# Kernel optimization log

Measured on AMD Instinct MI355X. Metric: run time of the kernel, lower is better.

The kernel has to match this reference:

```python
import jax, jax.numpy as jnp
import numpy as np

EMBED_DIM = 1024
N1 = 4096
N2 = 4096


def setup_inputs() -> dict:
    key = jax.random.key(0)
    ks = jax.random.split(key, 14)
    s = 1.0 / np.sqrt(EMBED_DIM)
    def lin(k):
        kw, kb = jax.random.split(k)
        W = jax.random.uniform(kw, (EMBED_DIM, EMBED_DIM), jnp.float32, -s, s)
        b = jax.random.uniform(kb, (EMBED_DIM,), jnp.float32, -s, s)
        return W, b
    Wq1, bq1 = lin(ks[0]); Wk1, bk1 = lin(ks[1]); Wv1, bv1 = lin(ks[2])
    Wq2, bq2 = lin(ks[3]); Wk2, bk2 = lin(ks[4]); Wv2, bv2 = lin(ks[5])
    x1 = jax.random.normal(ks[6], (N1, EMBED_DIM), jnp.float32)
    x2 = jax.random.normal(ks[7], (N2, EMBED_DIM), jnp.float32)
    return {
        "input_tensor1": x1, "input_tensor2": x2,
        "Wq1": Wq1, "bq1": bq1, "Wk1": Wk1, "bk1": bk1, "Wv1": Wv1, "bv1": bv1,
        "Wq2": Wq2, "bq2": bq2, "Wk2": Wk2, "bk2": bk2, "Wv2": Wv2, "bv2": bv2,
    }


def reference(input_tensor1, input_tensor2,
              Wq1, bq1, Wk1, bk1, Wv1, bv1,
              Wq2, bq2, Wk2, bk2, Wv2, bv2):
    scale = 1.0 / jnp.sqrt(jnp.asarray(EMBED_DIM, input_tensor1.dtype))
    # torch Linear: y = x @ W.T + b
    q1 = input_tensor1 @ Wq1.T + bq1   # [N1, D]
    k1 = input_tensor1 @ Wk1.T + bk1
    v1 = input_tensor1 @ Wv1.T + bv1
    q2 = input_tensor2 @ Wq2.T + bq2   # [N2, D]
    k2 = input_tensor2 @ Wk2.T + bk2
    v2 = input_tensor2 @ Wv2.T + bv2
    # stream-2 queries attend over stream-1 keys/values
    scores1 = (q2 @ k1.T) * scale                  # [N2, N1]
    probs1 = jax.nn.softmax(scores1, axis=-1)      # dropout p=0 -> identity
    context1 = probs1 @ v1                         # [N2, D]
    # stream-1 queries attend over stream-2 keys/values
    scores2 = (q1 @ k2.T) * scale                  # [N1, N2]
    probs2 = jax.nn.softmax(scores2, axis=-1)
    context2 = probs2 @ v2                         # [N1, D]
    return (context1, context2)
```

## Files before the change

kernel.cpp:

```cpp
#include <hip/hip_runtime.h>
#include <hip/hip_bf16.h>
#include <cstdint>
#include <cstddef>

#define DEVINL __device__ __forceinline__

typedef __attribute__((ext_vector_type(4))) float   f32x4;
typedef __bf16 bf16x8 __attribute__((ext_vector_type(8)));
typedef __attribute__((ext_vector_type(4))) short   short4v;
typedef __attribute__((ext_vector_type(4))) float   float4v;

static constexpr int DIM = 1024;
static constexpr int NTOK = 4096;

DEVINL unsigned short f2bf(float f) {
  unsigned u = __float_as_uint(f);
  u += 0x7FFF + ((u >> 16) & 1);
  return (unsigned short)(u >> 16);
}
DEVINL float bf2f(unsigned short s) {
  return __uint_as_float(((unsigned)s) << 16);
}

DEVINL void gll16(const void* g, void* l) {
  __builtin_amdgcn_global_load_lds(
      (const __attribute__((address_space(1))) void*)g,
      (__attribute__((address_space(3))) void*)l, 16, 0, 0);
}

struct B3 { int bx, by, bz; };
DEVINL B3 xcd_remap(int GX, int GY, int GZ) {
  const int flat = blockIdx.x + GX * (blockIdx.y + GY * blockIdx.z);
  const int nwg  = GX * GY * GZ;
  const int chunk = nwg >> 3;
  const int vbid = (flat & 7) * chunk + (flat >> 3);
  B3 r;
  r.bx = vbid % GX;
  r.by = (vbid / GX) % GY;
  r.bz = vbid / (GX * GY);
  return r;
}

DEVINL void core256x128(const unsigned short* __restrict__ A, int lda,
                        const unsigned short* __restrict__ B, int ldb,
                        int K, int brow, int bcol, f32x4 acc[4][4])
{
  __shared__ unsigned short lds[73728];
  const int t = threadIdx.x;
  const int w = t >> 6, l = t & 63;
  const int wr = w >> 1, wc = w & 1;
  const int l15 = l & 15;
  const int scol = ((l & 3) ^ ((l >> 3) & 3)) << 3;
  const int cs   = (((l >> 4) ^ ((l15 >> 1) & 3)) << 3);

  const unsigned short* aL = A + (size_t)(brow * 256 + w * 16 + (l >> 2)) * lda + scol;
  const unsigned short* bL = B + (size_t)(bcol * 128 + w * 16 + (l >> 2)) * ldb + scol;

#pragma unroll
  for (int m = 0; m < 4; ++m)
#pragma unroll
    for (int n = 0; n < 4; ++n) {
      f32x4 z = {0.f, 0.f, 0.f, 0.f};
      acc[m][n] = z;
    }

#define STAGE(buf, kt)                                                         \
  {                                                                            \
    gll16(aL + (size_t)(kt) * 32,                                              \
          lds + (buf) * 12288 + w * 512);                                      \
    gll16(aL + (size_t)128 * lda + (size_t)(kt) * 32,                          \
          lds + (buf) * 12288 + 4096 + w * 512);                               \
    gll16(bL + (size_t)(kt) * 32,                                              \
          lds + (buf) * 12288 + 8192 + w * 512);                               \
  }

  const int NT = K >> 5;

  STAGE(0, 0); STAGE(1, 1); STAGE(2, 2); STAGE(3, 3);

  bf16x8 af[4], bfv[4];
  int cur = 0;
  for (int kt = 0; kt < NT; ++kt) {
    int st = cur + 4; if (st >= 6) st -= 6;
    if (kt + 4 < NT) STAGE(st, kt + 4);

    const int rem = NT - 1 - kt;
    if (rem >= 4)      asm volatile("s_waitcnt vmcnt(12)" ::: "memory");
    else if (rem == 3) asm volatile("s_waitcnt vmcnt(9)"  ::: "memory");
    else if (rem == 2) asm volatile("s_waitcnt vmcnt(6)"  ::: "memory");
    else if (rem == 1) asm volatile("s_waitcnt vmcnt(3)"  ::: "memory");
    else               asm volatile("s_waitcnt vmcnt(0)"  ::: "memory");
    asm volatile("" ::: "memory");
    __builtin_amdgcn_s_barrier();
    asm volatile("" ::: "memory");

    const unsigned short* base = lds + cur * 12288;
#pragma unroll
    for (int m = 0; m < 4; ++m)
      af[m] = *(const bf16x8*)(base + (wr * 64 + m * 16 + l15) * 32 + cs);
#pragma unroll
    for (int n = 0; n < 4; ++n)
      bfv[n] = *(const bf16x8*)(base + 8192 + (wc * 64 + n * 16 + l15) * 32 + cs);

    __builtin_amdgcn_s_setprio(1);
#pragma unroll
    for (int m = 0; m < 4; ++m)
#pragma unroll
      for (int n = 0; n < 4; ++n)
        acc[m][n] = __builtin_amdgcn_mfma_f32_16x16x32_bf16(af[m], bfv[n], acc[m][n], 0, 0, 0);
    __builtin_amdgcn_s_setprio(0);

    cur = (cur + 1 == 6) ? 0 : cur + 1;
  }
#undef STAGE
}

__global__ __launch_bounds__(512, 2)
void gemm_scores(const unsigned short* __restrict__ A,
                 const unsigned short* __restrict__ B,
                 unsigned short* __restrict__ S, float scale)
{
  const B3 b = xcd_remap(32, 16, 1);
  f32x4 acc[4][4];
  core256x128(A, DIM, B, DIM, DIM, b.by, b.bx, acc);

  const int t = threadIdx.x, w = t >> 6, l = t & 63;
  const int wr = w >> 1, wc = w & 1;
  const int rr = (l >> 4) * 4, cc = l & 15;
#pragma unroll
  for (int m = 0; m < 4; ++m) {
    const int row0 = b.by * 256 + wr * 64 + m * 16 + rr;
#pragma unroll
    for (int n = 0; n < 4; ++n) {
      const int col = b.bx * 128 + wc * 64 + n * 16 + cc;
#pragma unroll
      for (int i = 0; i < 4; ++i)
        S[(size_t)(row0 + i) * NTOK + col] = f2bf(acc[m][n][i] * scale);
    }
  }
}

__global__ __launch_bounds__(512, 2)
void qkv_gemm(const unsigned short* __restrict__ x1, const unsigned short* __restrict__ x2,
              const unsigned short* __restrict__ W6,
              const float* bq1, const float* bk1, const float* bv1,
              const float* bq2, const float* bk2, const float* bv2,
              unsigned short* q1, unsigned short* k1, unsigned short* v1T,
              unsigned short* q2, unsigned short* k2, unsigned short* v2T)
{
  const B3 b = xcd_remap(8, 16, 6);
  const int g = b.bz;
  const unsigned short* A = (g < 3) ? x1 : x2;
  const unsigned short* W = W6 + (size_t)g * (DIM * DIM);
  const float* bias = (g == 0) ? bq1 : (g == 1) ? bk1 : (g == 2) ? bv1
                    : (g == 3) ? bq2 : (g == 4) ? bk2 : bv2;
  unsigned short* out = (g == 0) ? q1 : (g == 1) ? k1 : (g == 2) ? v1T
                      : (g == 3) ? q2 : (g == 4) ? k2 : v2T;
  const bool vT = (g == 2 || g == 5);

  f32x4 acc[4][4];
  core256x128(A, DIM, W, DIM, DIM, b.by, b.bx, acc);

  const int t = threadIdx.x, w = t >> 6, l = t & 63;
  const int wr = w >> 1, wc = w & 1;
  const int rr = (l >> 4) * 4, cc = l & 15;

  if (!vT) {
#pragma unroll
    for (int m = 0; m < 4; ++m) {
      const int row0 = b.by * 256 + wr * 64 + m * 16 + rr;
#pragma unroll
      for (int n = 0; n < 4; ++n) {
        const int col = b.bx * 128 + wc * 64 + n * 16 + cc;
        const float bv_ = bias[col];
#pragma unroll
        for (int i = 0; i < 4; ++i)
          out[(size_t)(row0 + i) * DIM + col] = f2bf(acc[m][n][i] + bv_);
      }
    }
  } else {
#pragma unroll
    for (int m = 0; m < 4; ++m) {
      const int row0 = b.by * 256 + wr * 64 + m * 16 + rr;
#pragma unroll
      for (int n = 0; n < 4; ++n) {
        const int col = b.bx * 128 + wc * 64 + n * 16 + cc;
        const float bv_ = bias[col];
        short4v pk;
#pragma unroll
        for (int i = 0; i < 4; ++i) pk[i] = (short)f2bf(acc[m][n][i] + bv_);
        *(short4v*)(out + (size_t)col * NTOK + row0) = pk;
      }
    }
  }
}

__global__ __launch_bounds__(512, 2)
void pv_gemm(const unsigned short* __restrict__ S1,
             const unsigned short* __restrict__ S2,
             const unsigned short* __restrict__ vTcat,
             float* __restrict__ out)
{
  const B3 b = xcd_remap(16, 16, 1);
  const int bx = b.bx, by = b.by;
  const unsigned short* A = (bx < 8) ? S1 : S2;

  f32x4 acc[4][4];
  core256x128(A, NTOK, vTcat, NTOK, NTOK, by, bx, acc);

  const int t = threadIdx.x, w = t >> 6, l = t & 63;
  const int wr = w >> 1, wc = w & 1;
  const int rr = (l >> 4) * 4, cc = l & 15;
#pragma unroll
  for (int m = 0; m < 4; ++m) {
    const int row0 = by * 256 + wr * 64 + m * 16 + rr;
#pragma unroll
    for (int n = 0; n < 4; ++n) {
      const int cg = bx * 128 + wc * 64 + n * 16 + cc;
      float* dstBase = (cg < 1024) ? (out + cg) : (out + 4194304 + (cg - 1024));
#pragma unroll
      for (int i = 0; i < 4; ++i)
        dstBase[(size_t)(row0 + i) * 1024] = acc[m][n][i];
    }
  }
}

__global__ __launch_bounds__(256)
void softmax_inplace(unsigned short* __restrict__ S)
{
  const int row = blockIdx.x;
  unsigned short* r = S + (size_t)row * NTOK;
  const int t = threadIdx.x, wave = t >> 6, lane = t & 63;
  __shared__ float red[4];

  bf16x8 d0 = *(const bf16x8*)(r + t * 8);
  bf16x8 d1 = *(const bf16x8*)(r + 2048 + t * 8);
  float v[16];
  {
    const unsigned short* p0 = (const unsigned short*)&d0;
    const unsigned short* p1 = (const unsigned short*)&d1;
#pragma unroll
    for (int j = 0; j < 8; ++j) { v[j] = bf2f(p0[j]); v[8 + j] = bf2f(p1[j]); }
  }
  float mx = v[0];
#pragma unroll
  for (int j = 1; j < 16; ++j) mx = fmaxf(mx, v[j]);
#pragma unroll
  for (int o = 32; o > 0; o >>= 1) mx = fmaxf(mx, __shfl_xor(mx, o));
  if (lane == 0) red[wave] = mx;
  __syncthreads();
  mx = fmaxf(fmaxf(red[0], red[1]), fmaxf(red[2], red[3]));

  float s = 0.f;
#pragma unroll
  for (int j = 0; j < 16; ++j) { v[j] = __expf(v[j] - mx); s += v[j]; }
#pragma unroll
  for (int o = 32; o > 0; o >>= 1) s += __shfl_xor(s, o);
  __syncthreads();
  if (lane == 0) red[wave] = s;
  __syncthreads();
  s = red[0] + red[1] + red[2] + red[3];
  const float inv = 1.0f / s;

  unsigned short o0[8], o1[8];
#pragma unroll
  for (int j = 0; j < 8; ++j) { o0[j] = f2bf(v[j] * inv); o1[j] = f2bf(v[8 + j] * inv); }
  *(bf16x8*)(r + t * 8)        = *(const bf16x8*)o0;
  *(bf16x8*)(r + 2048 + t * 8) = *(const bf16x8*)o1;
}

__global__ __launch_bounds__(256)
void cvt2(const float* __restrict__ a, const float* __restrict__ b,
          unsigned short* __restrict__ oa, unsigned short* __restrict__ ob)
{
  const float* in = blockIdx.y ? b : a;
  unsigned short* out = blockIdx.y ? ob : oa;
  const size_t i = ((size_t)blockIdx.x * 256 + threadIdx.x) * 4;
  float4v x = *(const float4v*)(in + i);
  short4v o;
#pragma unroll
  for (int j = 0; j < 4; ++j) o[j] = (short)f2bf(x[j]);
  *(short4v*)(out + i) = o;
}

__global__ __launch_bounds__(256)
void cvt_w(const float* w0, const float* w1, const float* w2,
           const float* w3, const float* w4, const float* w5,
           unsigned short* __restrict__ W6)
{
  const float* srcs[6] = {w0, w1, w2, w3, w4, w5};
  const float* in = srcs[blockIdx.y];
  unsigned short* out = W6 + (size_t)blockIdx.y * (DIM * DIM);
  const size_t i = ((size_t)blockIdx.x * 256 + threadIdx.x) * 4;
  float4v x = *(const float4v*)(in + i);
  short4v o;
#pragma unroll
  for (int j = 0; j < 4; ++j) o[j] = (short)f2bf(x[j]);
  *(short4v*)(out + i) = o;
}

extern "C" void kernel_launch(void* const* d_in, const int* in_sizes, int n_in,
                              void* d_out, int out_size, void* d_ws, size_t ws_size,
                              hipStream_t stream)
{
  const float* x1  = (const float*)d_in[0];
  const float* x2  = (const float*)d_in[1];
  const float* Wq1 = (const float*)d_in[2];  const float* bq1 = (const float*)d_in[3];
  const float* Wk1 = (const float*)d_in[4];  const float* bk1 = (const float*)d_in[5];
  const float* Wv1 = (const float*)d_in[6];  const float* bv1 = (const float*)d_in[7];
  const float* Wq2 = (const float*)d_in[8];  const float* bq2 = (const float*)d_in[9];
  const float* Wk2 = (const float*)d_in[10]; const float* bk2 = (const float*)d_in[11];
  const float* Wv2 = (const float*)d_in[12]; const float* bv2 = (const float*)d_in[13];
  float* out = (float*)d_out;

  unsigned short* ws  = (unsigned short*)d_ws;
  const size_t NTD = (size_t)NTOK * DIM;
  const size_t SM  = (size_t)NTOK * NTOK;
  unsigned short* x1b = ws;
  unsigned short* x2b = x1b + NTD;
  unsigned short* W6  = x2b + NTD;
  unsigned short* S1  = ws;
  unsigned short* S2  = ws + SM;
  unsigned short* q1  = ws + 2 * SM;
  unsigned short* k1  = q1 + NTD;
  unsigned short* q2  = k1 + NTD;
  unsigned short* k2  = q2 + NTD;
  unsigned short* vT  = k2 + NTD;
  unsigned short* v1T = vT;
  unsigned short* v2T = vT + NTD;

  const dim3 blk(256);
  cvt2 <<<dim3(NTD / 1024, 2), blk, 0, stream>>>(x1, x2, x1b, x2b);
  cvt_w<<<dim3((DIM * DIM) / 1024, 6), blk, 0, stream>>>(Wq1, Wk1, Wv1, Wq2, Wk2, Wv2, W6);

  qkv_gemm<<<dim3(8, 16, 6), dim3(512), 0, stream>>>(
      x1b, x2b, W6, bq1, bk1, bv1, bq2, bk2, bv2, q1, k1, v1T, q2, k2, v2T);

  const float scale = 0.03125f;

  gemm_scores<<<dim3(32, 16), dim3(512), 0, stream>>>(q2, k1, S1, scale);
  softmax_inplace<<<dim3(NTOK), blk, 0, stream>>>(S1);
  gemm_scores<<<dim3(32, 16), dim3(512), 0, stream>>>(q1, k2, S2, scale);
  softmax_inplace<<<dim3(NTOK), blk, 0, stream>>>(S2);

  pv_gemm<<<dim3(16, 16), dim3(512), 0, stream>>>(S1, S2, vT, out);
}
```

Baseline: 277.0 us.

## Use 256x256 tiled GEMM core with split-phase pipeline for QKV and scores

```diff
diff --git a/kernel.cpp b/kernel.cpp
--- a/kernel.cpp
+++ b/kernel.cpp
@@ -41,6 +41,125 @@
   return r;
 }
 
+DEVINL void core256v2(const unsigned short* __restrict__ A, int lda,
+                      const unsigned short* __restrict__ B, int ldb,
+                      int K, int brow, int bcol, f32x4 acc[8][4])
+{
+  __shared__ unsigned short lds[65536];
+  const int t = threadIdx.x;
+  const int w = t >> 6, l = t & 63;
+  const int wr = w >> 2, wc = w & 3;
+  const int srow = l >> 3;
+  const int scol = ((l & 7) ^ srow) << 3;
+  const int l15 = l & 15;
+  const int cs0 = (((l >> 4) << 3)        ^ ((l & 7) << 3));
+  const int cs1 = ((32 + ((l >> 4) << 3)) ^ ((l & 7) << 3));
+
+  const unsigned short* aL = A + (size_t)(brow * 256 + srow) * lda + scol;
+  const unsigned short* bL = B + (size_t)(bcol * 256 + srow) * ldb + scol;
+
+#pragma unroll
+  for (int m = 0; m < 8; ++m)
+#pragma unroll
+    for (int n = 0; n < 4; ++n) {
+      f32x4 z = {0.f, 0.f, 0.f, 0.f};
+      acc[m][n] = z;
+    }
+
+#define STA_(Sbase, h, r, kt)                                                  \
+  gll16(aL + (size_t)((r)*128 + (h)*64 + (w << 3)) * lda + (size_t)(kt)*64,    \
+        lds + (Sbase) + ((r)*128 + (h)*64 + (w << 3)) * 64)
+#define STB_(Sbase, h, r, kt)                                                  \
+  { const int g16_ = w + (r)*8;                                                \
+    const int r0_ = (g16_ >> 2)*64 + (h)*32 + (g16_ & 3)*8;                    \
+    gll16(bL + (size_t)r0_ * ldb + (size_t)(kt)*64, lds + (Sbase) + r0_ * 64); }
+#define LDA_(Abase, mh)                                                        \
+  _Pragma("unroll")                                                            \
+  for (int m4 = 0; m4 < 4; ++m4) {                                             \
+    const unsigned short* p_ = lds + (Abase) + (wr*128 + (mh)*64 + m4*16 + l15)*64; \
+    af[m4][0] = *(const bf16x8*)(p_ + cs0);                                    \
+    af[m4][1] = *(const bf16x8*)(p_ + cs1);                                    \
+  }
+#define LDB_(Bbase, nh)                                                        \
+  _Pragma("unroll")                                                            \
+  for (int n2 = 0; n2 < 2; ++n2) {                                             \
+    const unsigned short* p_ = lds + (Bbase) + (wc*64 + (nh)*32 + n2*16 + l15)*64;  \
+    bfr[n2][0] = *(const bf16x8*)(p_ + cs0);                                   \
+    bfr[n2][1] = *(const bf16x8*)(p_ + cs1);                                   \
+  }
+#define MF_(mh, nh)                                                            \
+  __builtin_amdgcn_s_setprio(1);                                               \
+  _Pragma("unroll")                                                            \
+  for (int m4 = 0; m4 < 4; ++m4)                                               \
+  _Pragma("unroll")                                                            \
+  for (int n2 = 0; n2 < 2; ++n2) {                                             \
+    f32x4 c_ = acc[(mh)*4 + m4][(nh)*2 + n2];                                  \
+    c_ = __builtin_amdgcn_mfma_f32_16x16x32_bf16(af[m4][0], bfr[n2][0], c_, 0,0,0); \
+    c_ = __builtin_amdgcn_mfma_f32_16x16x32_bf16(af[m4][1], bfr[n2][1], c_, 0,0,0); \
+    acc[(mh)*4 + m4][(nh)*2 + n2] = c_;                                        \
+  }                                                                            \
+  __builtin_amdgcn_s_setprio(0);
+#define VMW4() asm volatile("s_waitcnt vmcnt(4)" ::: "memory")
+#define VMW0() asm volatile("s_waitcnt vmcnt(0)" ::: "memory")
+#define BARR() do { asm volatile("" ::: "memory");                             \
+                    __builtin_amdgcn_s_barrier();                              \
+                    asm volatile("" ::: "memory"); } while (0)
+
+  STA_(0, 0, 0, 0); STA_(0, 0, 1, 0); STB_(16384, 0, 0, 0); STB_(16384, 0, 1, 0);
+  STA_(0, 1, 0, 0); STA_(0, 1, 1, 0); STB_(16384, 1, 0, 0); STB_(16384, 1, 1, 0);
+
+  bf16x8 af[4][2], bfr[2][2];
+  const int NT = K >> 6;
+  for (int kt = 0; kt < NT - 1; ++kt) {
+    const int Ab = (kt & 1) * 32768;
+    const int Bb = Ab + 16384;
+    const int Sa = ((kt & 1) ^ 1) * 32768;
+    const int Sb = Sa + 16384;
+
+    VMW4(); BARR();
+    STA_(Sa, 0, 0, kt + 1); STA_(Sa, 0, 1, kt + 1);
+    STB_(Sb, 0, 0, kt + 1); STB_(Sb, 0, 1, kt + 1);
+    LDA_(Ab, 0); LDB_(Bb, 0);
+    MF_(0, 0);
+
+    VMW4(); BARR();
+    STA_(Sa, 1, 0, kt + 1); STA_(Sa, 1, 1, kt + 1);
+    STB_(Sb, 1, 0, kt + 1); STB_(Sb, 1, 1, kt + 1);
+    LDA_(Ab, 1);
+    MF_(1, 0);
+
+    LDB_(Bb, 1);
+    MF_(1, 1);
+
+    LDA_(Ab, 0);
+    MF_(0, 1);
+  }
+
+  {
+    const int kt = NT - 1;
+    const int Ab = (kt & 1) * 32768;
+    const int Bb = Ab + 16384;
+    VMW4(); BARR();
+    LDA_(Ab, 0); LDB_(Bb, 0);
+    MF_(0, 0);
+    VMW0(); BARR();
+    LDA_(Ab, 1);
+    MF_(1, 0);
+    LDB_(Bb, 1);
+    MF_(1, 1);
+    LDA_(Ab, 0);
+    MF_(0, 1);
+  }
+#undef STA_
+#undef STB_
+#undef LDA_
+#undef LDB_
+#undef MF_
+#undef VMW4
+#undef VMW0
+#undef BARR
+}
+
 DEVINL void core256x128(const unsigned short* __restrict__ A, int lda,
                         const unsigned short* __restrict__ B, int ldb,
                         int K, int brow, int bcol, f32x4 acc[4][4])
@@ -115,40 +234,39 @@
 #undef STAGE
 }
 
-__global__ __launch_bounds__(512, 2)
-void gemm_scores(const unsigned short* __restrict__ A,
-                 const unsigned short* __restrict__ B,
-                 unsigned short* __restrict__ S, float scale)
-{
-  const B3 b = xcd_remap(32, 16, 1);
-  f32x4 acc[4][4];
-  core256x128(A, DIM, B, DIM, DIM, b.by, b.bx, acc);
+__global__ __launch_bounds__(512, 1)
+void gemm256_scores(const unsigned short* __restrict__ A,
+                    const unsigned short* __restrict__ B,
+                    unsigned short* __restrict__ S, float scale)
+{
+  const B3 b = xcd_remap(16, 16, 1);
+  f32x4 acc[8][4];
+  core256v2(A, DIM, B, DIM, DIM, b.by, b.bx, acc);
 
   const int t = threadIdx.x, w = t >> 6, l = t & 63;
-  const int wr = w >> 1, wc = w & 1;
-  const int rr = (l >> 4) * 4, cc = l & 15;
-#pragma unroll
-  for (int m = 0; m < 4; ++m) {
-    const int row0 = b.by * 256 + wr * 64 + m * 16 + rr;
-#pragma unroll
-    for (int n = 0; n < 4; ++n) {
-      const int col = b.bx * 128 + wc * 64 + n * 16 + cc;
+  const int wr = w >> 2, wc = w & 3;
+  const int r4 = (l >> 4) * 4, c = l & 15;
+  const int row0 = b.by * 256 + wr * 128;
+  const int col0 = b.bx * 256 + wc * 64;
+#pragma unroll
+  for (int mf = 0; mf < 8; ++mf)
+#pragma unroll
+    for (int nf = 0; nf < 4; ++nf)
 #pragma unroll
       for (int i = 0; i < 4; ++i)
-        S[(size_t)(row0 + i) * NTOK + col] = f2bf(acc[m][n][i] * scale);
-    }
-  }
-}
-
-__global__ __launch_bounds__(512, 2)
-void qkv_gemm(const unsigned short* __restrict__ x1, const unsigned short* __restrict__ x2,
-              const unsigned short* __restrict__ W6,
-              const float* bq1, const float* bk1, const float* bv1,
-              const float* bq2, const float* bk2, const float* bv2,
-              unsigned short* q1, unsigned short* k1, unsigned short* v1T,
-              unsigned short* q2, unsigned short* k2, unsigned short* v2T)
-{
-  const B3 b = xcd_remap(8, 16, 6);
+        S[(size_t)(row0 + mf*16 + r4 + i) * NTOK + col0 + nf*16 + c] =
+            f2bf(acc[mf][nf][i] * scale);
+}
+
+__global__ __launch_bounds__(512, 1)
+void qkv256(const unsigned short* __restrict__ x1, const unsigned short* __restrict__ x2,
+            const unsigned short* __restrict__ W6,
+            const float* bq1, const float* bk1, const float* bv1,
+            const float* bq2, const float* bk2, const float* bv2,
+            unsigned short* q1, unsigned short* k1, unsigned short* v1T,
+            unsigned short* q2, unsigned short* k2, unsigned short* v2T)
+{
+  const B3 b = xcd_remap(4, 16, 6);
   const int g = b.bz;
   const unsigned short* A = (g < 3) ? x1 : x2;
   const unsigned short* W = W6 + (size_t)g * (DIM * DIM);
@@ -158,40 +276,38 @@
                       : (g == 3) ? q2 : (g == 4) ? k2 : v2T;
   const bool vT = (g == 2 || g == 5);
 
-  f32x4 acc[4][4];
-  core256x128(A, DIM, W, DIM, DIM, b.by, b.bx, acc);
+  f32x4 acc[8][4];
+  core256v2(A, DIM, W, DIM, DIM, b.by, b.bx, acc);
 
   const int t = threadIdx.x, w = t >> 6, l = t & 63;
-  const int wr = w >> 1, wc = w & 1;
-  const int rr = (l >> 4) * 4, cc = l & 15;
+  const int wr = w >> 2, wc = w & 3;
+  const int r4 = (l >> 4) * 4, c = l & 15;
+  const int row0 = b.by * 256 + wr * 128;
+  const int col0 = b.bx * 256 + wc * 64;
+
+  float bias_v[4];
+#pragma unroll
+  for (int nf = 0; nf < 4; ++nf) bias_v[nf] = bias[col0 + nf*16 + c];
 
   if (!vT) {
 #pragma unroll
-    for (int m = 0; m < 4; ++m) {
-      const int row0 = b.by * 256 + wr * 64 + m * 16 + rr;
-#pragma unroll
-      for (int n = 0; n < 4; ++n) {
-        const int col = b.bx * 128 + wc * 64 + n * 16 + cc;
-        const float bv_ = bias[col];
+    for (int mf = 0; mf < 8; ++mf)
+#pragma unroll
+      for (int nf = 0; nf < 4; ++nf)
 #pragma unroll
         for (int i = 0; i < 4; ++i)
-          out[(size_t)(row0 + i) * DIM + col] = f2bf(acc[m][n][i] + bv_);
+          out[(size_t)(row0 + mf*16 + r4 + i) * DIM + col0 + nf*16 + c] =
+              f2bf(acc[mf][nf][i] + bias_v[nf]);
+  } else {
+#pragma unroll
+    for (int mf = 0; mf < 8; ++mf)
+#pragma unroll
+      for (int nf = 0; nf < 4; ++nf) {
+        short4v pk;
+#pragma unroll
+        for (int i = 0; i < 4; ++i) pk[i] = (short)f2bf(acc[mf][nf][i] + bias_v[nf]);
+        *(short4v*)(out + (size_t)(col0 + nf*16 + c) * NTOK + row0 + mf*16 + r4) = pk;
       }
-    }
-  } else {
-#pragma unroll
-    for (int m = 0; m < 4; ++m) {
-      const int row0 = b.by * 256 + wr * 64 + m * 16 + rr;
-#pragma unroll
-      for (int n = 0; n < 4; ++n) {
-        const int col = b.bx * 128 + wc * 64 + n * 16 + cc;
-        const float bv_ = bias[col];
-        short4v pk;
-#pragma unroll
-        for (int i = 0; i < 4; ++i) pk[i] = (short)f2bf(acc[m][n][i] + bv_);
-        *(short4v*)(out + (size_t)col * NTOK + row0) = pk;
-      }
-    }
   }
 }
 
@@ -333,14 +449,14 @@
   cvt2 <<<dim3(NTD / 1024, 2), blk, 0, stream>>>(x1, x2, x1b, x2b);
   cvt_w<<<dim3((DIM * DIM) / 1024, 6), blk, 0, stream>>>(Wq1, Wk1, Wv1, Wq2, Wk2, Wv2, W6);
 
-  qkv_gemm<<<dim3(8, 16, 6), dim3(512), 0, stream>>>(
+  qkv256<<<dim3(4, 16, 6), dim3(512), 0, stream>>>(
       x1b, x2b, W6, bq1, bk1, bv1, bq2, bk2, bv2, q1, k1, v1T, q2, k2, v2T);
 
   const float scale = 0.03125f;
 
-  gemm_scores<<<dim3(32, 16), dim3(512), 0, stream>>>(q2, k1, S1, scale);
+  gemm256_scores<<<dim3(16, 16), dim3(512), 0, stream>>>(q2, k1, S1, scale);
   softmax_inplace<<<dim3(NTOK), blk, 0, stream>>>(S1);
-  gemm_scores<<<dim3(32, 16), dim3(512), 0, stream>>>(q1, k2, S2, scale);
+  gemm256_scores<<<dim3(16, 16), dim3(512), 0, stream>>>(q1, k2, S2, scale);
   softmax_inplace<<<dim3(NTOK), blk, 0, stream>>>(S2);
 
   pv_gemm<<<dim3(16, 16), dim3(512), 0, stream>>>(S1, S2, vT, out);
```

Result: faster. 246.5 us (-11.0%).
